# Kernel tuning notes

Measured on AMD Instinct MI355X. Metric: run time of the kernel, lower is better.

The kernel has to match this reference:

```python
import jax, jax.numpy as jnp
import numpy as np
from jax import lax

B, W, L, K = 256, 4096, 16, 8  # batch, nodes/level, levels, fan-in


def setup_inputs() -> dict:
    key = jax.random.key(0)
    ks = jax.random.split(key, 7)
    s = 1.0 / np.sqrt(K)  # torch nn.Linear default init scale
    observed_bits = jnp.round(jax.random.uniform(ks[0], (B, W))).astype(jnp.float32)
    prior_w = jax.random.uniform(ks[1], (W,), minval=-1.0, maxval=1.0)  # PriorNode Linear(1,1) weight
    prior_b = jax.random.uniform(ks[2], (W,), minval=-1.0, maxval=1.0)
    weights = jax.random.uniform(ks[3], (L - 1, W, K), minval=-s, maxval=s)  # per-node Linear(K,1)
    biases = jax.random.uniform(ks[4], (L - 1, W), minval=-s, maxval=s)
    # parents sorted DESCENDING per node: heap pops higher rv first, so inputs are
    # concatenated in descending parent-rv order in the original traversal.
    parents = -jnp.sort(-jax.random.randint(ks[5], (L - 1, W, K), 0, W), axis=-1)
    inv_mask = jax.random.randint(ks[6], (L - 1, W), 0, 2).astype(bool)  # True -> InvNode
    return {"observed_bits": observed_bits, "prior_w": prior_w, "prior_b": prior_b,
            "weights": weights, "biases": biases, "parents": parents, "inv_mask": inv_mask}


def reference(observed_bits, prior_w, prior_b, weights, biases, parents, inv_mask):
    # Observed level: PriorNode with num_parents=1 -> relu(w*bit + b), per node.  (B, W)
    h = jax.nn.relu(observed_bits * prior_w[None, :] + prior_b[None, :])

    def step(h, lvl):
        w, b, p, inv = lvl  # (W,K), (W,), (W,K) int, (W,) bool
        x = h[:, p]                                   # gather parent outputs -> (B, W, K)
        x = jnp.where(inv[:, None], 1.0 - x, x)       # InvNode applies fc(1 - x)
        h2 = jax.nn.relu(jnp.einsum('bnk,nk->bn', x, w) + b)  # per-node Linear(K,1)+ReLU
        return h2, None

    h, _ = lax.scan(step, h, (weights, biases, parents, inv_mask))
    return h  # (B, num_input_bits) == pred.squeeze() of the original
```

## Files before the change

### kernel.cpp

```cpp
#include <hip/hip_runtime.h>

#define WN 4096
#define BN 256
#define KN 8
#define NLVL 15
#define NTHR 1024
#define NPT (WN / NTHR)

__global__ __launch_bounds__(256) void prep_kernel(
    const float* __restrict__ wts, const float* __restrict__ bia,
    const int* __restrict__ par,   const int* __restrict__ inv,
    float4* __restrict__ Wp, uint4* __restrict__ Pp, float* __restrict__ Bz) {
  const int idx = blockIdx.x * 256 + threadIdx.x;
  const float4 w0 = *(const float4*)(wts + (size_t)idx * KN);
  const float4 w1 = *(const float4*)(wts + (size_t)idx * KN + 4);
  const int4   p0 = *(const int4*)(par + (size_t)idx * KN);
  const int4   p1 = *(const int4*)(par + (size_t)idx * KN + 4);
  const bool   iv = inv[idx] != 0;
  const float  ws = ((w0.x + w0.y) + (w0.z + w0.w)) + ((w1.x + w1.y) + (w1.z + w1.w));
  const float  s  = iv ? -1.0f : 1.0f;
  Wp[(size_t)idx * 2]     = make_float4(w0.x * s, w0.y * s, w0.z * s, w0.w * s);
  Wp[(size_t)idx * 2 + 1] = make_float4(w1.x * s, w1.y * s, w1.z * s, w1.w * s);
  uint4 pp;
  pp.x = (unsigned)p0.x | ((unsigned)p0.y << 16);
  pp.y = (unsigned)p0.z | ((unsigned)p0.w << 16);
  pp.z = (unsigned)p1.x | ((unsigned)p1.y << 16);
  pp.w = (unsigned)p1.z | ((unsigned)p1.w << 16);
  Pp[idx] = pp;
  Bz[idx] = iv ? bia[idx] + ws : bia[idx];
}

__global__ __launch_bounds__(NTHR) void fused_lds_kernel(
    const float* __restrict__ obs, const float* __restrict__ pw,
    const float* __restrict__ pb,  const float4* __restrict__ Wp,
    const uint4* __restrict__ Pp,  const float* __restrict__ Bz,
    float* __restrict__ out) {
  __shared__ float h[2][WN];
  const int    t = threadIdx.x;
  const size_t b = blockIdx.x;

  uint4 pp[2][NPT];
  float bz[2][NPT];

#pragma unroll
  for (int i = 0; i < NPT; ++i) {
    pp[0][i] = Pp[i * NTHR + t];
    bz[0][i] = Bz[i * NTHR + t];
  }
#pragma unroll
  for (int i = 0; i < NPT; ++i) {
    const int n = i * NTHR + t;
    h[0][n] = fmaxf(fmaf(obs[b * WN + n], pw[n], pb[n]), 0.0f);
  }
  __syncthreads();

#pragma unroll
  for (int l = 0; l < NLVL; ++l) {
    const int cb = l & 1;
    const int nb = cb ^ 1;
    const float* hc = h[l & 1];
    float*       hn = h[(l + 1) & 1];

    if (l + 1 < NLVL) {
#pragma unroll
      for (int i = 0; i < NPT; ++i) {
        const size_t nl = (size_t)(l + 1) * WN + i * NTHR + t;
        pp[nb][i] = Pp[nl];
        bz[nb][i] = Bz[nl];
      }
    }

    float4 w0[NPT], w1[NPT];
#pragma unroll
    for (int i = 0; i < NPT; ++i) {
      const size_t nl = (size_t)l * WN + i * NTHR + t;
      w0[i] = Wp[nl * 2];
      w1[i] = Wp[nl * 2 + 1];
    }

#pragma unroll
    for (int i = 0; i < NPT; ++i) {
      const uint4 p = pp[cb][i];
      const float x0 = hc[p.x & 0xffffu];
      const float x1 = hc[p.x >> 16];
      const float x2 = hc[p.y & 0xffffu];
      const float x3 = hc[p.y >> 16];
      const float x4 = hc[p.z & 0xffffu];
      const float x5 = hc[p.z >> 16];
      const float x6 = hc[p.w & 0xffffu];
      const float x7 = hc[p.w >> 16];
      float acc = bz[cb][i];
      acc = fmaf(x0, w0[i].x, acc);
      acc = fmaf(x1, w0[i].y, acc);
      acc = fmaf(x2, w0[i].z, acc);
      acc = fmaf(x3, w0[i].w, acc);
      acc = fmaf(x4, w1[i].x, acc);
      acc = fmaf(x5, w1[i].y, acc);
      acc = fmaf(x6, w1[i].z, acc);
      acc = fmaf(x7, w1[i].w, acc);
      hn[i * NTHR + t] = fmaxf(acc, 0.0f);
    }
    __syncthreads();
  }

#pragma unroll
  for (int i = 0; i < NPT; ++i) {
    const int n = i * NTHR + t;
    out[b * WN + n] = h[NLVL & 1][n];
  }
}

extern "C" void kernel_launch(void* const* d_in, const int* in_sizes, int n_in,
                              void* d_out, int out_size, void* d_ws, size_t ws_size,
                              hipStream_t stream) {
  const float* obs = (const float*)d_in[0];
  const float* pw  = (const float*)d_in[1];
  const float* pb  = (const float*)d_in[2];
  const float* wts = (const float*)d_in[3];
  const float* bia = (const float*)d_in[4];
  const int*   par = (const int*)d_in[5];
  const int*   inv = (const int*)d_in[6];
  float* out = (float*)d_out;

  char* ws = (char*)d_ws;
  float4* Wp = (float4*)ws;
  uint4*  Pp = (uint4*)(ws + (size_t)NLVL * WN * 32);
  float*  Bz = (float*)(ws + (size_t)NLVL * WN * 48);

  prep_kernel<<<(NLVL * WN) / 256, 256, 0, stream>>>(wts, bia, par, inv, Wp, Pp, Bz);
  fused_lds_kernel<<<BN, NTHR, 0, stream>>>(obs, pw, pb, Wp, Pp, Bz, out);
}
```

Before: 111.0 us.

## Reorder parent gather slots per wavefront to reduce LDS bank conflicts

The prep kernel now assigns each node's eight (parent, weight) pairs to gather slots with a greedy per-wavefront balancing pass. It uses LDS counters per bank and atomics so that, for each slot k, the 64 lanes spread their LDS reads across the 32 banks. Reordering the terms of the dot product leaves the result unchanged apart from floating-point summation order. The goal is fewer bank conflicts in the main kernel's gather from h. The cost is a heavier prep kernel with many syncthreads and atomics, and the balancing assumes one wave of 64 lanes per block. It also assumes the main kernel's wave-to-node mapping matches blocks of 64 consecutive nodes, which holds since lanes t in a 1024-thread block map contiguously.

```diff
diff --git a/kernel.cpp b/kernel.cpp
--- a/kernel.cpp
+++ b/kernel.cpp
@@ -7,27 +7,85 @@
 #define NTHR 1024
 #define NPT (WN / NTHR)
 
-__global__ __launch_bounds__(256) void prep_kernel(
+__global__ __launch_bounds__(64) void prep2_kernel(
     const float* __restrict__ wts, const float* __restrict__ bia,
     const int* __restrict__ par,   const int* __restrict__ inv,
     float4* __restrict__ Wp, uint4* __restrict__ Pp, float* __restrict__ Bz) {
-  const int idx = blockIdx.x * 256 + threadIdx.x;
-  const float4 w0 = *(const float4*)(wts + (size_t)idx * KN);
-  const float4 w1 = *(const float4*)(wts + (size_t)idx * KN + 4);
-  const int4   p0 = *(const int4*)(par + (size_t)idx * KN);
-  const int4   p1 = *(const int4*)(par + (size_t)idx * KN + 4);
+  __shared__ unsigned cnt[32];
+  const int lane = threadIdx.x;
+  const int idx  = blockIdx.x * 64 + lane;
+  const int4   pA = *(const int4*)(par + (size_t)idx * KN);
+  const int4   pB = *(const int4*)(par + (size_t)idx * KN + 4);
+  const float4 wA = *(const float4*)(wts + (size_t)idx * KN);
+  const float4 wB = *(const float4*)(wts + (size_t)idx * KN + 4);
   const bool   iv = inv[idx] != 0;
-  const float  ws = ((w0.x + w0.y) + (w0.z + w0.w)) + ((w1.x + w1.y) + (w1.z + w1.w));
+  const float  sw = ((wA.x + wA.y) + (wA.z + wA.w)) + ((wB.x + wB.y) + (wB.z + wB.w));
   const float  s  = iv ? -1.0f : 1.0f;
-  Wp[(size_t)idx * 2]     = make_float4(w0.x * s, w0.y * s, w0.z * s, w0.w * s);
-  Wp[(size_t)idx * 2 + 1] = make_float4(w1.x * s, w1.y * s, w1.z * s, w1.w * s);
-  uint4 pp;
-  pp.x = (unsigned)p0.x | ((unsigned)p0.y << 16);
-  pp.y = (unsigned)p0.z | ((unsigned)p0.w << 16);
-  pp.z = (unsigned)p1.x | ((unsigned)p1.y << 16);
-  pp.w = (unsigned)p1.z | ((unsigned)p1.w << 16);
-  Pp[idx] = pp;
-  Bz[idx] = iv ? bia[idx] + ws : bia[idx];
+  const int   p0 = pA.x, p1 = pA.y, p2 = pA.z, p3 = pA.w;
+  const int   p4 = pB.x, p5 = pB.y, p6 = pB.z, p7 = pB.w;
+  const float w0 = wA.x * s, w1 = wA.y * s, w2 = wA.z * s, w3 = wA.w * s;
+  const float w4 = wB.x * s, w5 = wB.y * s, w6 = wB.z * s, w7 = wB.w * s;
+
+  unsigned mask = 0xffu;
+  unsigned slotpack = 0;
+
+  for (int k = 0; k < KN; ++k) {
+    if (lane < 32) cnt[lane] = 0;
+    __syncthreads();
+    bool done = false;
+    for (int it = 0; it < 3; ++it) {
+      if (!done) {
+        unsigned bestj = 8, bestv = 0xffffffffu;
+#define SCAN(J, PJ) if (mask & (1u << (J))) { unsigned v = cnt[(PJ) & 31]; if (v < bestv) { bestv = v; bestj = (J); } }
+        SCAN(0, p0) SCAN(1, p1) SCAN(2, p2) SCAN(3, p3)
+        SCAN(4, p4) SCAN(5, p5) SCAN(6, p6) SCAN(7, p7)
+#undef SCAN
+        const unsigned bank =
+            (bestj == 0) ? (p0 & 31) : (bestj == 1) ? (p1 & 31) :
+            (bestj == 2) ? (p2 & 31) : (bestj == 3) ? (p3 & 31) :
+            (bestj == 4) ? (p4 & 31) : (bestj == 5) ? (p5 & 31) :
+            (bestj == 6) ? (p6 & 31) : (p7 & 31);
+        const unsigned cap = (it < 2) ? 2u : 3u;
+        const unsigned old = atomicAdd(&cnt[bank], 1u);
+        if (old < cap) {
+          slotpack |= (unsigned)k << (4u * bestj);
+          mask &= ~(1u << bestj);
+          done = true;
+        } else {
+          atomicAdd(&cnt[bank], (unsigned)-1);
+        }
+      }
+      __syncthreads();
+    }
+    if (!done) {
+      const unsigned bestj = (unsigned)__ffs(mask) - 1u;
+      slotpack |= (unsigned)k << (4u * bestj);
+      mask &= ~(1u << bestj);
+    }
+    __syncthreads();
+  }
+
+#define SLOT_OF(J) ((slotpack >> (4u * (J))) & 15u)
+#define PICKW(K) (SLOT_OF(0) == (K) ? w0 : SLOT_OF(1) == (K) ? w1 : \
+                  SLOT_OF(2) == (K) ? w2 : SLOT_OF(3) == (K) ? w3 : \
+                  SLOT_OF(4) == (K) ? w4 : SLOT_OF(5) == (K) ? w5 : \
+                  SLOT_OF(6) == (K) ? w6 : w7)
+#define PICKP(K) (unsigned)(SLOT_OF(0) == (K) ? p0 : SLOT_OF(1) == (K) ? p1 : \
+                  SLOT_OF(2) == (K) ? p2 : SLOT_OF(3) == (K) ? p3 : \
+                  SLOT_OF(4) == (K) ? p4 : SLOT_OF(5) == (K) ? p5 : \
+                  SLOT_OF(6) == (K) ? p6 : p7)
+  const float ow0 = PICKW(0), ow1 = PICKW(1), ow2 = PICKW(2), ow3 = PICKW(3);
+  const float ow4 = PICKW(4), ow5 = PICKW(5), ow6 = PICKW(6), ow7 = PICKW(7);
+  const unsigned op0 = PICKP(0), op1 = PICKP(1), op2 = PICKP(2), op3 = PICKP(3);
+  const unsigned op4 = PICKP(4), op5 = PICKP(5), op6 = PICKP(6), op7 = PICKP(7);
+#undef SLOT_OF
+#undef PICKW
+#undef PICKP
+  Pp[idx] = make_uint4(op0 | (op1 << 16), op2 | (op3 << 16),
+                       op4 | (op5 << 16), op6 | (op7 << 16));
+  Wp[(size_t)idx * 2]     = make_float4(ow0, ow1, ow2, ow3);
+  Wp[(size_t)idx * 2 + 1] = make_float4(ow4, ow5, ow6, ow7);
+  Bz[idx] = iv ? bia[idx] + sw : bia[idx];
 }
 
 __global__ __launch_bounds__(NTHR) void fused_lds_kernel(
@@ -127,6 +185,6 @@
   uint4*  Pp = (uint4*)(ws + (size_t)NLVL * WN * 32);
   float*  Bz = (float*)(ws + (size_t)NLVL * WN * 48);
 
-  prep_kernel<<<(NLVL * WN) / 256, 256, 0, stream>>>(wts, bia, par, inv, Wp, Pp, Bz);
+  prep2_kernel<<<(NLVL * WN) / 64, 64, 0, stream>>>(wts, bia, par, inv, Wp, Pp, Bz);
   fused_lds_kernel<<<BN, NTHR, 0, stream>>>(obs, pw, pb, Wp, Pp, Bz, out);
 }
```

Result: slower. 126.7 us (+14.1%).

## Reorder per-node parent gathers to spread LDS banks and store weights in fp16

Applied to the files above, without the earlier changes.

The prep kernel now greedily reorders each node's eight parent indices so that, at each gather step, the lanes of a wavefront hit LDS banks that are as evenly spread as possible. It uses per-wave shared counters and atomics to do this. Weights are also packed as fp16 pairs, which halves the per-level weight traffic the main kernel reads from global memory. The cost is a more expensive prep kernel with many syncthreads, plus reduced weight precision: the inverted-node bias folding still uses fp32 sums while the products use rounded fp16 weights, so accuracy may drift.

```diff
diff --git a/kernel.cpp b/kernel.cpp
--- a/kernel.cpp
+++ b/kernel.cpp
@@ -1,4 +1,5 @@
 #include <hip/hip_runtime.h>
+#include <hip/hip_fp16.h>
 
 #define WN 4096
 #define BN 256
@@ -10,29 +11,74 @@
 __global__ __launch_bounds__(256) void prep_kernel(
     const float* __restrict__ wts, const float* __restrict__ bia,
     const int* __restrict__ par,   const int* __restrict__ inv,
-    float4* __restrict__ Wp, uint4* __restrict__ Pp, float* __restrict__ Bz) {
-  const int idx = blockIdx.x * 256 + threadIdx.x;
-  const float4 w0 = *(const float4*)(wts + (size_t)idx * KN);
-  const float4 w1 = *(const float4*)(wts + (size_t)idx * KN + 4);
-  const int4   p0 = *(const int4*)(par + (size_t)idx * KN);
-  const int4   p1 = *(const int4*)(par + (size_t)idx * KN + 4);
+    uint4* __restrict__ Wh, uint4* __restrict__ Pp, float* __restrict__ Bz) {
+  __shared__ unsigned cnt[4][32];
+  const int t    = threadIdx.x;
+  const int wv   = t >> 6;
+  const int lane = t & 63;
+  const int idx  = blockIdx.x * 256 + t;
+  unsigned* c = cnt[wv];
+
+  const int4   pA = *(const int4*)(par + (size_t)idx * KN);
+  const int4   pB = *(const int4*)(par + (size_t)idx * KN + 4);
+  const float4 wA = *(const float4*)(wts + (size_t)idx * KN);
+  const float4 wB = *(const float4*)(wts + (size_t)idx * KN + 4);
   const bool   iv = inv[idx] != 0;
-  const float  ws = ((w0.x + w0.y) + (w0.z + w0.w)) + ((w1.x + w1.y) + (w1.z + w1.w));
+  const float  sw = ((wA.x + wA.y) + (wA.z + wA.w)) + ((wB.x + wB.y) + (wB.z + wB.w));
   const float  s  = iv ? -1.0f : 1.0f;
-  Wp[(size_t)idx * 2]     = make_float4(w0.x * s, w0.y * s, w0.z * s, w0.w * s);
-  Wp[(size_t)idx * 2 + 1] = make_float4(w1.x * s, w1.y * s, w1.z * s, w1.w * s);
-  uint4 pp;
-  pp.x = (unsigned)p0.x | ((unsigned)p0.y << 16);
-  pp.y = (unsigned)p0.z | ((unsigned)p0.w << 16);
-  pp.z = (unsigned)p1.x | ((unsigned)p1.y << 16);
-  pp.w = (unsigned)p1.z | ((unsigned)p1.w << 16);
-  Pp[idx] = pp;
-  Bz[idx] = iv ? bia[idx] + ws : bia[idx];
+  const int   p0 = pA.x, p1 = pA.y, p2 = pA.z, p3 = pA.w;
+  const int   p4 = pB.x, p5 = pB.y, p6 = pB.z, p7 = pB.w;
+  const float w0 = wA.x * s, w1 = wA.y * s, w2 = wA.z * s, w3 = wA.w * s;
+  const float w4 = wB.x * s, w5 = wB.y * s, w6 = wB.z * s, w7 = wB.w * s;
+
+  unsigned mask = 0xffu;
+  unsigned op[KN];
+  float    ow[KN];
+
+#pragma unroll
+  for (int k = 0; k < KN; ++k) {
+    __syncthreads();
+    if (lane < 32) c[lane] = 0;
+    __syncthreads();
+    unsigned bestj = 0, bestv = 0xffffffffu;
+#define SCAN(J, PJ) if (mask & (1u << (J))) { unsigned v = c[(PJ) & 31]; if (v < bestv) { bestv = v; bestj = (J); } }
+    SCAN(0, p0) SCAN(1, p1) SCAN(2, p2) SCAN(3, p3)
+    SCAN(4, p4) SCAN(5, p5) SCAN(6, p6) SCAN(7, p7)
+#undef SCAN
+    const unsigned pj =
+        (bestj == 0) ? (unsigned)p0 : (bestj == 1) ? (unsigned)p1 :
+        (bestj == 2) ? (unsigned)p2 : (bestj == 3) ? (unsigned)p3 :
+        (bestj == 4) ? (unsigned)p4 : (bestj == 5) ? (unsigned)p5 :
+        (bestj == 6) ? (unsigned)p6 : (unsigned)p7;
+    const float wj =
+        (bestj == 0) ? w0 : (bestj == 1) ? w1 :
+        (bestj == 2) ? w2 : (bestj == 3) ? w3 :
+        (bestj == 4) ? w4 : (bestj == 5) ? w5 :
+        (bestj == 6) ? w6 : w7;
+    atomicAdd(&c[pj & 31], 1u);
+    op[k] = pj;
+    ow[k] = wj;
+    mask &= ~(1u << bestj);
+  }
+
+  Pp[idx] = make_uint4(op[0] | (op[1] << 16), op[2] | (op[3] << 16),
+                       op[4] | (op[5] << 16), op[6] | (op[7] << 16));
+  uint4 wq;
+  wq.x = (unsigned)__half_as_ushort(__float2half(ow[0])) |
+         ((unsigned)__half_as_ushort(__float2half(ow[1])) << 16);
+  wq.y = (unsigned)__half_as_ushort(__float2half(ow[2])) |
+         ((unsigned)__half_as_ushort(__float2half(ow[3])) << 16);
+  wq.z = (unsigned)__half_as_ushort(__float2half(ow[4])) |
+         ((unsigned)__half_as_ushort(__float2half(ow[5])) << 16);
+  wq.w = (unsigned)__half_as_ushort(__float2half(ow[6])) |
+         ((unsigned)__half_as_ushort(__float2half(ow[7])) << 16);
+  Wh[idx] = wq;
+  Bz[idx] = iv ? bia[idx] + sw : bia[idx];
 }
 
 __global__ __launch_bounds__(NTHR) void fused_lds_kernel(
     const float* __restrict__ obs, const float* __restrict__ pw,
-    const float* __restrict__ pb,  const float4* __restrict__ Wp,
+    const float* __restrict__ pb,  const uint4* __restrict__ Wh,
     const uint4* __restrict__ Pp,  const float* __restrict__ Bz,
     float* __restrict__ out) {
   __shared__ float h[2][WN];
@@ -70,13 +116,10 @@
       }
     }
 
-    float4 w0[NPT], w1[NPT];
+    uint4 wq[NPT];
 #pragma unroll
-    for (int i = 0; i < NPT; ++i) {
-      const size_t nl = (size_t)l * WN + i * NTHR + t;
-      w0[i] = Wp[nl * 2];
-      w1[i] = Wp[nl * 2 + 1];
-    }
+    for (int i = 0; i < NPT; ++i)
+      wq[i] = Wh[(size_t)l * WN + i * NTHR + t];
 
 #pragma unroll
     for (int i = 0; i < NPT; ++i) {
@@ -89,15 +132,20 @@
       const float x5 = hc[p.z >> 16];
       const float x6 = hc[p.w & 0xffffu];
       const float x7 = hc[p.w >> 16];
+      const __half2* hw = reinterpret_cast<const __half2*>(&wq[i]);
+      const float2 f01 = __half22float2(hw[0]);
+      const float2 f23 = __half22float2(hw[1]);
+      const float2 f45 = __half22float2(hw[2]);
+      const float2 f67 = __half22float2(hw[3]);
       float acc = bz[cb][i];
-      acc = fmaf(x0, w0[i].x, acc);
-      acc = fmaf(x1, w0[i].y, acc);
-      acc = fmaf(x2, w0[i].z, acc);
-      acc = fmaf(x3, w0[i].w, acc);
-      acc = fmaf(x4, w1[i].x, acc);
-      acc = fmaf(x5, w1[i].y, acc);
-      acc = fmaf(x6, w1[i].z, acc);
-      acc = fmaf(x7, w1[i].w, acc);
+      acc = fmaf(x0, f01.x, acc);
+      acc = fmaf(x1, f01.y, acc);
+      acc = fmaf(x2, f23.x, acc);
+      acc = fmaf(x3, f23.y, acc);
+      acc = fmaf(x4, f45.x, acc);
+      acc = fmaf(x5, f45.y, acc);
+      acc = fmaf(x6, f67.x, acc);
+      acc = fmaf(x7, f67.y, acc);
       hn[i * NTHR + t] = fmaxf(acc, 0.0f);
     }
     __syncthreads();
@@ -123,10 +171,10 @@
   float* out = (float*)d_out;
 
   char* ws = (char*)d_ws;
-  float4* Wp = (float4*)ws;
-  uint4*  Pp = (uint4*)(ws + (size_t)NLVL * WN * 32);
-  float*  Bz = (float*)(ws + (size_t)NLVL * WN * 48);
+  uint4* Wh = (uint4*)ws;
+  uint4* Pp = (uint4*)(ws + (size_t)NLVL * WN * 16);
+  float* Bz = (float*)(ws + (size_t)NLVL * WN * 32);
 
-  prep_kernel<<<(NLVL * WN) / 256, 256, 0, stream>>>(wts, bia, par, inv, Wp, Pp, Bz);
-  fused_lds_kernel<<<BN, NTHR, 0, stream>>>(obs, pw, pb, Wp, Pp, Bz, out);
+  prep_kernel<<<(NLVL * WN) / 256, 256, 0, stream>>>(wts, bia, par, inv, Wh, Pp, Bz);
+  fused_lds_kernel<<<BN, NTHR, 0, stream>>>(obs, pw, pb, Wh, Pp, Bz, out);
 }
```

Result: faster. 106.0 us (-4.5%).
